# Kernel tuning notes

Measured on AMD Instinct MI355X. Metric: run time of the kernel, lower is better.

The kernel has to match this reference:

```python
import jax, jax.numpy as jnp
import numpy as np

IN_FEATURES = 1024
OUT_FEATURES = 1024
NUM_GRIDS = 8
GRID_MIN, GRID_MAX = -2.0, 2.0
DENOM = (GRID_MAX - GRID_MIN) / (NUM_GRIDS - 1)
LN_EPS = 1e-5
GRID = jnp.linspace(GRID_MIN, GRID_MAX, NUM_GRIDS)


def setup_inputs() -> dict:
    key = jax.random.key(0)
    k_x, k_sw, k_bw = jax.random.split(key, 3)
    N = 8192
    x = jax.random.normal(k_x, (N, IN_FEATURES), dtype=jnp.float32)
    ln_gamma = jnp.ones((IN_FEATURES,), dtype=jnp.float32)
    ln_beta = jnp.zeros((IN_FEATURES,), dtype=jnp.float32)
    # trunc_normal(std=0.1) approximated by scaled normal
    spline_w = 0.1 * jax.random.normal(k_sw, (OUT_FEATURES, IN_FEATURES * NUM_GRIDS), dtype=jnp.float32)
    base_w = jax.random.normal(k_bw, (OUT_FEATURES, IN_FEATURES), dtype=jnp.float32) * (1.0 / np.sqrt(IN_FEATURES))
    base_b = jnp.zeros((OUT_FEATURES,), dtype=jnp.float32)
    return {"x": x, "ln_gamma": ln_gamma, "ln_beta": ln_beta,
            "spline_w": spline_w, "base_w": base_w, "base_b": base_b}


def reference(x, ln_gamma, ln_beta, spline_w, base_w, base_b):
    # LayerNorm over last dim
    mu = jnp.mean(x, axis=-1, keepdims=True)
    var = jnp.var(x, axis=-1, keepdims=True)
    xn = (x - mu) * jax.lax.rsqrt(var + LN_EPS) * ln_gamma + ln_beta
    # RBF basis: [N, in, G]
    basis = jnp.exp(-jnp.square((xn[..., None] - GRID) / DENOM))
    basis = basis.reshape(x.shape[0], IN_FEATURES * NUM_GRIDS)
    y = jnp.einsum('nk,ok->no', basis, spline_w)
    y = y + jnp.einsum('nd,od->no', jax.nn.silu(x), base_w) + base_b
    return y
```

## Files before the change

kernel.cpp:

```cpp
#include <hip/hip_runtime.h>
#include <hip/hip_bf16.h>
#include <stdint.h>

#define IN_F 1024
#define OUT_F 1024
#define NG 8
#define KSPLINE 8192
#define KDIM 9216
#define KHALF 4608
#define M_ROWS 8192
#define LOG2E 1.4426950408889634f
#define KC 2.1019642153762872f
#define CQ0 (-2.0f * KC)
#define DQ  (0.5714285714285714f * KC)
#define DQ2 1.4426950408889634f
#define QCHAIN 0.1353352832366127f


#define A_BLOCKS (M_ROWS / 4)
#define WS_BLOCKS 4096
#define WSIL_BLOCKS 1024
#define RB (KDIM * 2)

using half4v = __attribute__((ext_vector_type(4))) _Float16;
using half8  = __attribute__((ext_vector_type(8))) _Float16;
using f32x4  = __attribute__((ext_vector_type(4))) float;

#define AS1 __attribute__((address_space(1)))
#define AS3 __attribute__((address_space(3)))

__device__ __forceinline__ half8 spline8c(float xq) {
    float d0 = xq - CQ0;
    float b  = __builtin_amdgcn_exp2f(-(d0 * d0));
    float r  = __builtin_amdgcn_exp2f(fmaf(2.0f * DQ, d0, -DQ2));
    half8 h;
#pragma unroll
    for (int g = 0; g < 8; ++g) {
        h[g] = (_Float16)b;
        if (g < 7) { b = b * r; r = r * QCHAIN; }
    }
    return h;
}

__global__ __launch_bounds__(256) void prep_kernel(
        const float* __restrict__ x, const float* __restrict__ gamma,
        const float* __restrict__ beta, const float* __restrict__ sw,
        const float* __restrict__ bw, _Float16* __restrict__ A,
        _Float16* __restrict__ W) {
    const int b = blockIdx.x;
    if (b >= A_BLOCKS + WS_BLOCKS) {
        int t = (b - A_BLOCKS - WS_BLOCKS) * 256 + threadIdx.x;
        int o = t >> 8, d4 = t & 255;
        f32x4 v = __builtin_nontemporal_load(&((const f32x4*)bw)[o * 256 + d4]);
        half4v h = { (_Float16)v.x, (_Float16)v.y, (_Float16)v.z, (_Float16)v.w };
        *(half4v*)(W + (size_t)o * KDIM + KSPLINE + d4 * 4) = h;
        return;
    }
    if (b >= A_BLOCKS) {
        int t = (b - A_BLOCKS) * 256 + threadIdx.x;
        int o = t >> 10, f = t & 1023;
        const f32x4* src = &((const f32x4*)sw)[((size_t)o * 1024 + f) * 2];
        f32x4 v0 = __builtin_nontemporal_load(src);
        f32x4 v1 = __builtin_nontemporal_load(src + 1);
        half8 h = { (_Float16)v0.x, (_Float16)v0.y, (_Float16)v0.z, (_Float16)v0.w,
                    (_Float16)v1.x, (_Float16)v1.y, (_Float16)v1.z, (_Float16)v1.w };
        int p8 = (f >> 8) * 256 + (f & 3) * 64 + ((f >> 2) & 63);
        *(half8*)(W + (size_t)o * KDIM + p8 * 8) = h;
        return;
    }
    const int wave = threadIdx.x >> 6, lane = threadIdx.x & 63;
    const int row = b * 4 + wave;
    const f32x4* xr4 = (const f32x4*)(x + (size_t)row * IN_F);

    f32x4 xv[4];
    float s = 0.0f, s2 = 0.0f;
#pragma unroll
    for (int j = 0; j < 4; ++j) {
        f32x4 v = xr4[j * 64 + lane];
        xv[j] = v;
        s  += v.x + v.y + v.z + v.w;
        s2 += v.x * v.x + v.y * v.y + v.z * v.z + v.w * v.w;
    }
#pragma unroll
    for (int off = 32; off > 0; off >>= 1) {
        s  += __shfl_xor(s, off);
        s2 += __shfl_xor(s2, off);
    }
    float mu   = s * (1.0f / IN_F);
    float var  = s2 * (1.0f / IN_F) - mu * mu;
    float rstd = rsqrtf(var + 1e-5f);

    _Float16* Arow = A + (size_t)row * KDIM;
    _Float16* silu_out = Arow + KSPLINE;
#pragma unroll
    for (int j = 0; j < 4; ++j) {
        int idx = j * 64 + lane;
        f32x4 g  = ((const f32x4*)gamma)[idx];
        f32x4 bt = ((const f32x4*)beta)[idx];
        float xs4[4] = { xv[j].x, xv[j].y, xv[j].z, xv[j].w };
        float gg[4]  = { g.x, g.y, g.z, g.w };
        float bb4[4] = { bt.x, bt.y, bt.z, bt.w };
        half4v sil;
#pragma unroll
        for (int c = 0; c < 4; ++c) {
            float xs = xs4[c];
            float xq = fmaf((xs - mu) * rstd, gg[c] * KC, bb4[c] * KC);
            half8 h = spline8c(xq);
            *(half8*)(Arow + (size_t)(j * 256 + c * 64 + lane) * 8) = h;
            sil[c] = (_Float16)(xs / (1.0f + exp2f(-xs * LOG2E)));
        }
        *(half4v*)(silu_out + idx * 4) = sil;
    }
}

__global__ __launch_bounds__(512, 2) void gemm_kernel(
        const _Float16* __restrict__ A, const _Float16* __restrict__ W,
        const float* __restrict__ bias, float* __restrict__ C,
        float* __restrict__ P, int ntiles, int gpz) {
    extern __shared__ __align__(16) char smem[];
    const int tid  = threadIdx.x;
    const int wave = tid >> 6, lane = tid & 63;
    const int wm = wave >> 2, wn = wave & 3;

    const int lb = blockIdx.x;
    const int per_xcd = gridDim.x >> 5;
    const int xcd = lb & 7, sl = lb >> 3;
    const int g  = xcd * per_xcd + (sl >> 2);
    const int bn = sl & 3;
    const int bm = g / gpz;
    const int z  = g - bm * gpz;

    const int l8 = lane >> 3;
    const int chunkswz = ((lane & 7) ^ l8) << 4;
    const size_t zoff = (size_t)z * (KHALF * 2);
    const int gA[4] = {0, 128, 64, 192};
    const int gB[4] = {0, 128, 32, 160};
    const char* pA[4];
    const char* pB[4];
#pragma unroll
    for (int s = 0; s < 4; ++s) {
        pA[s] = (const char*)A + (size_t)(bm * 256 + gA[s] + wave * 8 + l8) * RB
                + zoff + chunkswz;
        pB[s] = (const char*)W + (size_t)(bn * 256 + gB[s] + (wave >> 2) * 64
                + (wave & 3) * 8 + l8) * RB + zoff + chunkswz;
    }

#define STAGE_A(s, nb, colb) __builtin_amdgcn_global_load_lds( \
        (const AS1 void*)(pA[s] + (colb)), \
        (AS3 void*)(smem + (nb) + (s) * 8192 + wave * 1024), 16, 0, 0)
#define STAGE_B(s, nb, colb) __builtin_amdgcn_global_load_lds( \
        (const AS1 void*)(pB[s] + (colb)), \
        (AS3 void*)(smem + (nb) + 32768 + (s) * 8192 + wave * 1024), 16, 0, 0)

    const int lm  = lane & 15;
    const int hi  = (lane >> 4) << 4;
    const int swz = (lm & 7) << 4;
    const int ck0 = (0  + hi) ^ swz;
    const int ck1 = (64 + hi) ^ swz;
    const int aB0 = (0 + wm) * 8192 + lm * 128;
    const int aB1 = (2 + wm) * 8192 + lm * 128;
    const int bB0 = 32768 + (0 + (wn >> 1)) * 8192 + ((wn & 1) * 32 + lm) * 128;
    const int bB1 = 32768 + (2 + (wn >> 1)) * 8192 + ((wn & 1) * 32 + lm) * 128;

    f32x4 acc[8][4] = {};
    half8 aF[4][2], bF[2][2], aG[4][2], bG[2][2];

#define MFMA8(MB, NB2, Aa, Bb, KH)                                              \
    _Pragma("unroll")                                                           \
    for (int n = 0; n < 2; ++n)                                                 \
        _Pragma("unroll")                                                       \
        for (int m = 0; m < 4; ++m)                                             \
            acc[(MB)+m][(NB2)+n] = __builtin_amdgcn_mfma_f32_16x16x32_f16(      \
                Aa[m][KH], Bb[n][KH], acc[(MB)+m][(NB2)+n], 0, 0, 0);

    STAGE_A(0, 0, 0); STAGE_A(1, 0, 0);
    STAGE_B(0, 0, 0); STAGE_B(1, 0, 0);
    STAGE_B(2, 0, 0); STAGE_B(3, 0, 0);
    STAGE_A(2, 0, 0); STAGE_A(3, 0, 0);
    asm volatile("s_waitcnt vmcnt(4)" ::: "memory");
    __builtin_amdgcn_s_barrier();
#pragma unroll
    for (int m = 0; m < 4; ++m) {
        aF[m][0] = *(const half8*)(smem + aB0 + m * 2048 + ck0);
        aF[m][1] = *(const half8*)(smem + aB0 + m * 2048 + ck1);
    }
#pragma unroll
    for (int n = 0; n < 2; ++n) {
        bF[n][0] = *(const half8*)(smem + bB0 + n * 2048 + ck0);
        bF[n][1] = *(const half8*)(smem + bB0 + n * 2048 + ck1);
    }

    for (int kt = 0; kt < ntiles; ++kt) {
        const int cb = (kt & 1) * 65536;
        const int nb = cb ^ 65536;
        const size_t col = (size_t)(kt + 1) * 128;
        const bool pref = (kt + 1 < ntiles);

        asm volatile("s_waitcnt vmcnt(2)" ::: "memory");
        if (pref) { STAGE_A(0, nb, col); STAGE_A(1, nb, col); }
        __builtin_amdgcn_s_barrier();
        asm volatile("s_waitcnt lgkmcnt(0)" ::: "memory");
        __builtin_amdgcn_s_setprio(1);
        MFMA8(0, 0, aF, bF, 0)
#pragma unroll
        for (int n = 0; n < 2; ++n) {
            bG[n][0] = *(const half8*)(smem + cb + bB1 + n * 2048 + ck0);
            bG[n][1] = *(const half8*)(smem + cb + bB1 + n * 2048 + ck1);
        }
        MFMA8(0, 0, aF, bF, 1)
        __builtin_amdgcn_s_setprio(0);
        __builtin_amdgcn_s_barrier();

        if (pref) {
            asm volatile("s_waitcnt vmcnt(2)" ::: "memory");
            STAGE_B(0, nb, col); STAGE_B(1, nb, col);
        } else {
            asm volatile("s_waitcnt vmcnt(0)" ::: "memory");
        }
        __builtin_amdgcn_s_barrier();
        asm volatile("s_waitcnt lgkmcnt(0)" ::: "memory");
        __builtin_amdgcn_s_setprio(1);
        MFMA8(0, 2, aF, bG, 0)
#pragma unroll
        for (int m = 0; m < 4; ++m) {
            aG[m][0] = *(const half8*)(smem + cb + aB1 + m * 2048 + ck0);
            aG[m][1] = *(const half8*)(smem + cb + aB1 + m * 2048 + ck1);
        }
        MFMA8(0, 2, aF, bG, 1)
        __builtin_amdgcn_s_setprio(0);
        __builtin_amdgcn_s_barrier();

        if (pref) { STAGE_B(2, nb, col); STAGE_B(3, nb, col); }
        __builtin_amdgcn_s_barrier();
        asm volatile("s_waitcnt lgkmcnt(0)" ::: "memory");
        __builtin_amdgcn_s_setprio(1);
        MFMA8(4, 0, aG, bF, 0)
        MFMA8(4, 0, aG, bF, 1)
        __builtin_amdgcn_s_setprio(0);
        __builtin_amdgcn_s_barrier();

        if (pref) {
            asm volatile("s_waitcnt vmcnt(2)" ::: "memory");
            STAGE_A(2, nb, col); STAGE_A(3, nb, col);
        } else {
            asm volatile("s_waitcnt vmcnt(0)" ::: "memory");
        }
        __builtin_amdgcn_s_barrier();
        asm volatile("s_waitcnt lgkmcnt(0)" ::: "memory");
        __builtin_amdgcn_s_setprio(1);
        MFMA8(4, 2, aG, bG, 0)
        if (pref) {
#pragma unroll
            for (int m = 0; m < 4; ++m) {
                aF[m][0] = *(const half8*)(smem + nb + aB0 + m * 2048 + ck0);
                aF[m][1] = *(const half8*)(smem + nb + aB0 + m * 2048 + ck1);
            }
#pragma unroll
            for (int n = 0; n < 2; ++n) {
                bF[n][0] = *(const half8*)(smem + nb + bB0 + n * 2048 + ck0);
                bF[n][1] = *(const half8*)(smem + nb + bB0 + n * 2048 + ck1);
            }
        }
        MFMA8(4, 2, aG, bG, 1)
        __builtin_amdgcn_s_setprio(0);
        __builtin_amdgcn_s_barrier();
    }

    const int cn  = lane & 15;
    const int rm4 = (lane >> 4) * 4;
    float* dst = z ? P : C;
#pragma unroll
    for (int nf = 0; nf < 4; ++nf) {
        int col = bn * 256 + wn * 64 + nf * 16 + cn;
        float bv = z ? 0.0f : bias[col];
#pragma unroll
        for (int mf = 0; mf < 8; ++mf) {
            int row = bm * 256 + wm * 128 + mf * 16 + rm4;
            float* cp = dst + (size_t)row * OUT_F + col;
#pragma unroll
            for (int r = 0; r < 4; ++r)
                cp[(size_t)r * OUT_F] = acc[mf][nf][r] + bv;
        }
    }
}

__global__ __launch_bounds__(256) void reduce_kernel(float* __restrict__ C,
        const float* __restrict__ P) {
    const int n4 = M_ROWS * OUT_F / 4;
    float4* c4 = (float4*)C;
    const float4* p4 = (const float4*)P;
    for (int i = blockIdx.x * 256 + threadIdx.x; i < n4; i += 2048 * 256) {
        float4 a = c4[i];
        float4 b = p4[i];
        a.x += b.x; a.y += b.y; a.z += b.z; a.w += b.w;
        c4[i] = a;
    }
}

extern "C" void kernel_launch(void* const* d_in, const int* in_sizes, int n_in,
                              void* d_out, int out_size, void* d_ws, size_t ws_size,
                              hipStream_t stream) {
    const float* x     = (const float*)d_in[0];
    const float* gamma = (const float*)d_in[1];
    const float* beta  = (const float*)d_in[2];
    const float* sw    = (const float*)d_in[3];
    const float* bw    = (const float*)d_in[4];
    const float* bb    = (const float*)d_in[5];
    float* out = (float*)d_out;

    char* ws = (char*)d_ws;
    size_t offW = 0;
    size_t offA = (size_t)OUT_F * KDIM * 2;
    size_t offP = offA + (size_t)M_ROWS * KDIM * 2;
    size_t need = offP + (size_t)M_ROWS * OUT_F * 4;
    _Float16* Wb = (_Float16*)(ws + offW);
    _Float16* Ab = (_Float16*)(ws + offA);
    float*    Pb = (float*)(ws + offP);
    const int split = (ws_size >= need);

    static int s_attr = 0;
    if (!s_attr) {
        (void)hipFuncSetAttribute(reinterpret_cast<const void*>(gemm_kernel),
                            hipFuncAttributeMaxDynamicSharedMemorySize, 131072);
        s_attr = 1;
    }

    prep_kernel<<<A_BLOCKS + WS_BLOCKS + WSIL_BLOCKS, 256, 0, stream>>>(
        x, gamma, beta, sw, bw, Ab, Wb);
    if (split) {
        gemm_kernel<<<256, 512, 131072, stream>>>(Ab, Wb, bb, out, Pb, KHALF / 64, 2);
        reduce_kernel<<<2048, 256, 0, stream>>>(out, Pb);
    } else {
        gemm_kernel<<<128, 512, 131072, stream>>>(Ab, Wb, bb, out, Pb, KDIM / 64, 1);
    }
}
```

Measured before the change: 283.2 us.

## Deepen GEMM main loop to prefetch two K-tiles ahead with in-place refill

Restructures the fp16 MFMA GEMM main loop so global-to-LDS loads run two tiles ahead instead of one. Both LDS buffers are filled in the prologue, and each phase refills the slice of the current buffer it has just finished reading. Fragment register loads move to the start of each phase rather than being interleaved with the MFMAs, and the loop is peeled into a macro with per-phase vmcnt thresholds plus two drain iterations. The aim is to hide more global memory latency. The risk is that LDS reads are no longer overlapped with MFMA issue, and the hand-tuned waitcnt values could hide races.

Result: no change. 282.1 us (-0.4%).

```diff
diff --git a/kernel.cpp b/kernel.cpp
--- a/kernel.cpp
+++ b/kernel.cpp
@@ -163,7 +163,6 @@
     const int bB1 = 32768 + (2 + (wn >> 1)) * 8192 + ((wn & 1) * 32 + lm) * 128;
 
     f32x4 acc[8][4] = {};
-    half8 aF[4][2], bF[2][2], aG[4][2], bG[2][2];
 
 #define MFMA8(MB, NB2, Aa, Bb, KH)                                              \
     _Pragma("unroll")                                                           \
@@ -173,98 +172,92 @@
             acc[(MB)+m][(NB2)+n] = __builtin_amdgcn_mfma_f32_16x16x32_f16(      \
                 Aa[m][KH], Bb[n][KH], acc[(MB)+m][(NB2)+n], 0, 0, 0);
 
+#define VMW_(n) asm volatile("s_waitcnt vmcnt(" #n ")" ::: "memory")
+#define VMW(n)  VMW_(n)
+
+#define GTILE(kt, W0, W1, W3, STG)                                              \
+{                                                                               \
+    const int cb = ((kt) & 1) * 65536;                                          \
+    const size_t col2 = (size_t)((kt) + 2) * 128;                               \
+    half8 aF[4][2], bF[2][2];                                                   \
+                  \
+    _Pragma("unroll")                                                           \
+    for (int m = 0; m < 4; ++m) {                                               \
+        aF[m][0] = *(const half8*)(smem + cb + aB0 + m * 2048 + ck0);           \
+        aF[m][1] = *(const half8*)(smem + cb + aB0 + m * 2048 + ck1);           \
+    }                                                                           \
+    _Pragma("unroll")                                                           \
+    for (int n = 0; n < 2; ++n) {                                               \
+        bF[n][0] = *(const half8*)(smem + cb + bB0 + n * 2048 + ck0);           \
+        bF[n][1] = *(const half8*)(smem + cb + bB0 + n * 2048 + ck1);           \
+    }                                                                           \
+    VMW(W0);                                                                    \
+    asm volatile("s_waitcnt lgkmcnt(8)" ::: "memory");                          \
+    __builtin_amdgcn_s_barrier();                                               \
+    asm volatile("s_waitcnt lgkmcnt(0)" ::: "memory");                          \
+    __builtin_amdgcn_s_setprio(1);                                              \
+    MFMA8(0, 0, aF, bF, 0)                                                      \
+    MFMA8(0, 0, aF, bF, 1)                                                      \
+    __builtin_amdgcn_s_setprio(0);                                              \
+    __builtin_amdgcn_s_barrier();                                               \
+      \
+    half8 bG[2][2];                                                             \
+    _Pragma("unroll")                                                           \
+    for (int n = 0; n < 2; ++n) {                                               \
+        bG[n][0] = *(const half8*)(smem + cb + bB1 + n * 2048 + ck0);           \
+        bG[n][1] = *(const half8*)(smem + cb + bB1 + n * 2048 + ck1);           \
+    }                                                                           \
+    VMW(W1);                                                                    \
+    if (STG) { STAGE_A(0, cb, col2); STAGE_A(1, cb, col2);                      \
+               STAGE_B(0, cb, col2); STAGE_B(1, cb, col2); }                    \
+    __builtin_amdgcn_s_barrier();                                               \
+    asm volatile("s_waitcnt lgkmcnt(0)" ::: "memory");                          \
+    __builtin_amdgcn_s_setprio(1);                                              \
+    MFMA8(0, 2, aF, bG, 0)                                                      \
+    MFMA8(0, 2, aF, bG, 1)                                                      \
+    __builtin_amdgcn_s_setprio(0);                                              \
+    __builtin_amdgcn_s_barrier();                                               \
+                             \
+    half8 aG[4][2];                                                             \
+    _Pragma("unroll")                                                           \
+    for (int m = 0; m < 4; ++m) {                                               \
+        aG[m][0] = *(const half8*)(smem + cb + aB1 + m * 2048 + ck0);           \
+        aG[m][1] = *(const half8*)(smem + cb + aB1 + m * 2048 + ck1);           \
+    }                                                                           \
+    if (STG) { STAGE_B(2, cb, col2); STAGE_B(3, cb, col2); }                    \
+    __builtin_amdgcn_s_barrier();                                               \
+    asm volatile("s_waitcnt lgkmcnt(0)" ::: "memory");                          \
+    __builtin_amdgcn_s_setprio(1);                                              \
+    MFMA8(4, 0, aG, bF, 0)                                                      \
+    MFMA8(4, 0, aG, bF, 1)                                                      \
+    __builtin_amdgcn_s_setprio(0);                                              \
+    __builtin_amdgcn_s_barrier();                                               \
+                 \
+    if (STG) { STAGE_A(2, cb, col2); STAGE_A(3, cb, col2); }                    \
+    VMW(W3);                                                                    \
+    __builtin_amdgcn_s_barrier();                                               \
+    __builtin_amdgcn_s_setprio(1);                                              \
+    MFMA8(4, 2, aG, bG, 0)                                                      \
+    MFMA8(4, 2, aG, bG, 1)                                                      \
+    __builtin_amdgcn_s_setprio(0);                                              \
+    __builtin_amdgcn_s_barrier();                                               \
+}
+
     STAGE_A(0, 0, 0); STAGE_A(1, 0, 0);
     STAGE_B(0, 0, 0); STAGE_B(1, 0, 0);
     STAGE_B(2, 0, 0); STAGE_B(3, 0, 0);
     STAGE_A(2, 0, 0); STAGE_A(3, 0, 0);
-    asm volatile("s_waitcnt vmcnt(4)" ::: "memory");
+    STAGE_A(0, 65536, 128); STAGE_A(1, 65536, 128);
+    STAGE_B(0, 65536, 128); STAGE_B(1, 65536, 128);
+    STAGE_B(2, 65536, 128); STAGE_B(3, 65536, 128);
+    STAGE_A(2, 65536, 128); STAGE_A(3, 65536, 128);
+    VMW(12);
     __builtin_amdgcn_s_barrier();
-#pragma unroll
-    for (int m = 0; m < 4; ++m) {
-        aF[m][0] = *(const half8*)(smem + aB0 + m * 2048 + ck0);
-        aF[m][1] = *(const half8*)(smem + aB0 + m * 2048 + ck1);
-    }
-#pragma unroll
-    for (int n = 0; n < 2; ++n) {
-        bF[n][0] = *(const half8*)(smem + bB0 + n * 2048 + ck0);
-        bF[n][1] = *(const half8*)(smem + bB0 + n * 2048 + ck1);
-    }
-
-    for (int kt = 0; kt < ntiles; ++kt) {
-        const int cb = (kt & 1) * 65536;
-        const int nb = cb ^ 65536;
-        const size_t col = (size_t)(kt + 1) * 128;
-        const bool pref = (kt + 1 < ntiles);
-
-        asm volatile("s_waitcnt vmcnt(2)" ::: "memory");
-        if (pref) { STAGE_A(0, nb, col); STAGE_A(1, nb, col); }
-        __builtin_amdgcn_s_barrier();
-        asm volatile("s_waitcnt lgkmcnt(0)" ::: "memory");
-        __builtin_amdgcn_s_setprio(1);
-        MFMA8(0, 0, aF, bF, 0)
-#pragma unroll
-        for (int n = 0; n < 2; ++n) {
-            bG[n][0] = *(const half8*)(smem + cb + bB1 + n * 2048 + ck0);
-            bG[n][1] = *(const half8*)(smem + cb + bB1 + n * 2048 + ck1);
-        }
-        MFMA8(0, 0, aF, bF, 1)
-        __builtin_amdgcn_s_setprio(0);
-        __builtin_amdgcn_s_barrier();
-
-        if (pref) {
-            asm volatile("s_waitcnt vmcnt(2)" ::: "memory");
-            STAGE_B(0, nb, col); STAGE_B(1, nb, col);
-        } else {
-            asm volatile("s_waitcnt vmcnt(0)" ::: "memory");
-        }
-        __builtin_amdgcn_s_barrier();
-        asm volatile("s_waitcnt lgkmcnt(0)" ::: "memory");
-        __builtin_amdgcn_s_setprio(1);
-        MFMA8(0, 2, aF, bG, 0)
-#pragma unroll
-        for (int m = 0; m < 4; ++m) {
-            aG[m][0] = *(const half8*)(smem + cb + aB1 + m * 2048 + ck0);
-            aG[m][1] = *(const half8*)(smem + cb + aB1 + m * 2048 + ck1);
-        }
-        MFMA8(0, 2, aF, bG, 1)
-        __builtin_amdgcn_s_setprio(0);
-        __builtin_amdgcn_s_barrier();
-
-        if (pref) { STAGE_B(2, nb, col); STAGE_B(3, nb, col); }
-        __builtin_amdgcn_s_barrier();
-        asm volatile("s_waitcnt lgkmcnt(0)" ::: "memory");
-        __builtin_amdgcn_s_setprio(1);
-        MFMA8(4, 0, aG, bF, 0)
-        MFMA8(4, 0, aG, bF, 1)
-        __builtin_amdgcn_s_setprio(0);
-        __builtin_amdgcn_s_barrier();
-
-        if (pref) {
-            asm volatile("s_waitcnt vmcnt(2)" ::: "memory");
-            STAGE_A(2, nb, col); STAGE_A(3, nb, col);
-        } else {
-            asm volatile("s_waitcnt vmcnt(0)" ::: "memory");
-        }
-        __builtin_amdgcn_s_barrier();
-        asm volatile("s_waitcnt lgkmcnt(0)" ::: "memory");
-        __builtin_amdgcn_s_setprio(1);
-        MFMA8(4, 2, aG, bG, 0)
-        if (pref) {
-#pragma unroll
-            for (int m = 0; m < 4; ++m) {
-                aF[m][0] = *(const half8*)(smem + nb + aB0 + m * 2048 + ck0);
-                aF[m][1] = *(const half8*)(smem + nb + aB0 + m * 2048 + ck1);
-            }
-#pragma unroll
-            for (int n = 0; n < 2; ++n) {
-                bF[n][0] = *(const half8*)(smem + nb + bB0 + n * 2048 + ck0);
-                bF[n][1] = *(const half8*)(smem + nb + bB0 + n * 2048 + ck1);
-            }
-        }
-        MFMA8(4, 2, aG, bG, 1)
-        __builtin_amdgcn_s_setprio(0);
-        __builtin_amdgcn_s_barrier();
-    }
+
+    for (int kt = 0; kt < ntiles - 2; ++kt)
+        GTILE(kt, 10, 8, 12, true)
+    GTILE(ntiles - 2, 10, 8, 4, false)
+    GTILE(ntiles - 1, 2, 0, 0, false)
 
     const int cn  = lane & 15;
     const int rm4 = (lane >> 4) * 4;
```
